# Performance work log

Measured on AMD Instinct MI355X. Metric: run time of the kernel, lower is better.

Reference implementation:

```python
import jax, jax.numpy as jnp
import numpy as np

B, S, D = 2, 2048, 1024
H, HD, K = 16, 64, 4
F = 4096
EPS = 1e-6
ROPE_BASE = 10000.0
NEG = -1e9


def rmsnorm(x, w):
    return x * jax.lax.rsqrt(jnp.mean(x * x, axis=-1, keepdims=True) + EPS) * w


def rope(t, pos):
    # t: (B,S,H,HD), pos: (B,S,H) per-node position (float)
    inv_freq = 1.0 / (ROPE_BASE ** (jnp.arange(0, HD, 2, dtype=jnp.float32) / HD))
    ang = pos[..., None] * inv_freq  # (B,S,H,HD/2)
    cos, sin = jnp.cos(ang), jnp.sin(ang)
    t1, t2 = t[..., : HD // 2], t[..., HD // 2:]
    return jnp.concatenate([t1 * cos - t2 * sin, t2 * cos + t1 * sin], axis=-1)


def setup_inputs() -> dict:
    key = jax.random.key(0)
    ks = jax.random.split(key, 12)
    s = lambda d: 1.0 / np.sqrt(d)
    return {
        "x": jax.random.normal(ks[0], (B, S, D), jnp.float32),
        "attn_norm_w": jnp.ones((D,), jnp.float32),
        "ffn_norm_w": jnp.ones((D,), jnp.float32),
        "Wq": jax.random.normal(ks[1], (D, H * HD), jnp.float32) * s(D),
        "Wk": jax.random.normal(ks[2], (D, H * HD), jnp.float32) * s(D),
        "Wv": jax.random.normal(ks[3], (D, H * HD), jnp.float32) * s(D),
        "Wo": jax.random.normal(ks[4], (H * HD, D), jnp.float32) * s(H * HD),
        "Wr": jax.random.normal(ks[5], (D, H * K), jnp.float32) * s(D),
        "w1": jax.random.normal(ks[6], (D, F), jnp.float32) * s(D),
        "w2": jax.random.normal(ks[7], (D, F), jnp.float32) * s(D),
        "w3": jax.random.normal(ks[8], (F, D), jnp.float32) * s(F),
    }


def reference(x, attn_norm_w, ffn_norm_w, Wq, Wk, Wv, Wo, Wr, w1, w2, w3):
    # ---- pre-norm + hypergraph node-routed causal attention ----
    h = rmsnorm(x, attn_norm_w)
    # per-(token, head) routing to K hyper-nodes
    logits = (h @ Wr).reshape(B, S, H, K)
    node = jnp.argmax(logits, axis=-1)                      # (B,S,H) int
    onehot = jax.nn.one_hot(node, K, dtype=jnp.float32)     # (B,S,H,K)
    # per-node RoPE position: count of previous same-node tokens
    cum = jnp.cumsum(onehot, axis=1)                        # inclusive
    pos = jnp.take_along_axis(cum, node[..., None], axis=-1)[..., 0] - 1.0  # (B,S,H)

    q = (h @ Wq).reshape(B, S, H, HD)
    k = (h @ Wk).reshape(B, S, H, HD)
    v = (h @ Wv).reshape(B, S, H, HD)
    q = rope(q, pos)
    k = rope(k, pos)

    scores = jnp.einsum("bqhd,bkhd->bhqk", q, k) / np.sqrt(HD)  # (B,H,S,S)
    node_h = jnp.transpose(node, (0, 2, 1))                     # (B,H,S)
    same = node_h[:, :, :, None] == node_h[:, :, None, :]       # intra-node only
    causal = jnp.tril(jnp.ones((S, S), bool))
    allowed = same & causal
    attn = jax.nn.softmax(jnp.where(allowed, scores, NEG), axis=-1)
    ctx = jnp.einsum("bhqk,bkhd->bqhd", attn, v).reshape(B, S, H * HD)
    x = x + ctx @ Wo

    # ---- pre-norm + SwiGLU ----
    h2 = rmsnorm(x, ffn_norm_w)
    ffn = (jax.nn.silu(h2 @ w1) * (h2 @ w2)) @ w3
    return x + ffn
```

## Files before the change

### kernel.cpp

```cpp
#include <hip/hip_runtime.h>
#include <hip/hip_bf16.h>
#include <math.h>

typedef __hip_bfloat16 bf16;

#define B_  2
#define S_  2048
#define D_  1024
#define H_  16
#define HD_ 64
#define KR_ 4
#define F_  4096
#define TOK (B_*S_)
#define NEG (-1.0e9f)

typedef __attribute__((ext_vector_type(8))) short bf16x8_t;
typedef __attribute__((ext_vector_type(4))) float f32x4_t;
typedef unsigned int u32;
#define AS1 __attribute__((address_space(1)))
#define AS3 __attribute__((address_space(3)))

__device__ __forceinline__ float u2f(unsigned short u) {
  union { float f; unsigned int i; } cv; cv.i = ((unsigned int)u) << 16; return cv.f;
}
__device__ __forceinline__ unsigned short f2u(float f) {
  return (unsigned short)(__bfloat16_as_ushort(__float2bfloat16(f)));
}

__device__ __forceinline__ void gl_lds16(const bf16* g, unsigned short* lds_base) {
  __builtin_amdgcn_global_load_lds((const AS1 u32*)g, (AS3 u32*)lds_base, 16, 0, 0);
}

__device__ __forceinline__ float rd1(const void* p, size_t i, bool isbf) {
  return isbf ? __bfloat162float(((const bf16*)p)[i]) : ((const float*)p)[i];
}

__device__ __forceinline__ void xcd_tile(int& bx, int& by) {
  const int nx = gridDim.x;
  const int nwg = nx * gridDim.y;
  const int hw = blockIdx.y * nx + blockIdx.x;
  const int tile = (hw & 7) * (nwg >> 3) + (hw >> 3);
  bx = tile % nx;
  by = tile / nx;
}

__global__ void detect_k(const unsigned* __restrict__ anw_words, int* __restrict__ flag) {
  if (threadIdx.x == 0) *flag = (anw_words[0] == 0x3F803F80u) ? 1 : 0;
}

__global__ __launch_bounds__(256) void transpose_k(const void* W, bf16* __restrict__ WT,
                                                   const int* __restrict__ flagp,
                                                   int K, int N) {
  const bool isbf = (*flagp != 0);
  __shared__ float tile[32][33];
  const int k0 = blockIdx.y * 32, n0 = blockIdx.x * 32;
  const int tid = threadIdx.x;
  const int rl = tid >> 5, cl = tid & 31;
#pragma unroll
  for (int i = 0; i < 4; i++)
    tile[rl + 8 * i][cl] = rd1(W, (size_t)(k0 + rl + 8 * i) * N + n0 + cl, isbf);
  __syncthreads();
#pragma unroll
  for (int i = 0; i < 4; i++)
    WT[(size_t)(n0 + rl + 8 * i) * K + k0 + cl] = __float2bfloat16(tile[cl][rl + 8 * i]);
}

__global__ __launch_bounds__(256) void wrconv_k(const void* Wr, float* __restrict__ Wrf,
                                                const int* __restrict__ flagp) {
  const bool isbf = (*flagp != 0);
  const int i = blockIdx.x * 256 + threadIdx.x;
  Wrf[i] = rd1(Wr, i, isbf);
}

template <bool XDUAL, bool WF>
__global__ __launch_bounds__(256) void rmsnorm_k(const void* x, const void* w,
                                                 bf16* __restrict__ ob,
                                                 float* __restrict__ of,
                                                 const int* __restrict__ flagp) {
  const bool isbf = (*flagp != 0);
  const int row = blockIdx.x;
  const int t = threadIdx.x;
  float v[4];
  float ss = 0.f;
#pragma unroll
  for (int i = 0; i < 4; i++) {
    const size_t idx = (size_t)row * D_ + t + 256 * i;
    v[i] = XDUAL ? rd1(x, idx, isbf) : ((const float*)x)[idx];
    ss += v[i] * v[i];
  }
#pragma unroll
  for (int off = 32; off >= 1; off >>= 1) ss += __shfl_down(ss, off);
  __shared__ float red[4];
  if ((t & 63) == 0) red[t >> 6] = ss;
  __syncthreads();
  const float tot = red[0] + red[1] + red[2] + red[3];
  const float sc = rsqrtf(tot * (1.f / D_) + 1e-6f);
#pragma unroll
  for (int i = 0; i < 4; i++) {
    const int c = t + 256 * i;
    const float r = v[i] * sc * rd1(w, c, isbf);
    ob[(size_t)row * D_ + c] = __float2bfloat16(r);
    if (WF) of[(size_t)row * D_ + c] = r;
  }
}

__global__ __launch_bounds__(256) void router_k(const float* __restrict__ h,
                                                const float* __restrict__ Wrf,
                                                int* __restrict__ node) {
  const int tok0 = blockIdx.x * 16;
  const int t = threadIdx.x;
  __shared__ float hs[16][1024];
  __shared__ float lg[16][64];
  {
    const float4* hsrc = (const float4*)(h + (size_t)tok0 * D_);
    float4* hdst = (float4*)hs;
#pragma unroll
    for (int j = 0; j < 16; j++) hdst[j * 256 + t] = hsrc[j * 256 + t];
  }
  __syncthreads();
  const int col = t & 63, tg = t >> 6;
  float acc[4] = {0.f, 0.f, 0.f, 0.f};
  for (int i = 0; i < D_; i += 4) {
    float wv[4];
#pragma unroll
    for (int u = 0; u < 4; u++) wv[u] = Wrf[(size_t)(i + u) * 64 + col];
#pragma unroll
    for (int tt = 0; tt < 4; tt++) {
      const float4 hv = *(const float4*)&hs[tg * 4 + tt][i];
      acc[tt] = fmaf(hv.x, wv[0], acc[tt]);
      acc[tt] = fmaf(hv.y, wv[1], acc[tt]);
      acc[tt] = fmaf(hv.z, wv[2], acc[tt]);
      acc[tt] = fmaf(hv.w, wv[3], acc[tt]);
    }
  }
#pragma unroll
  for (int tt = 0; tt < 4; tt++) lg[tg * 4 + tt][col] = acc[tt];
  __syncthreads();
  const int tok = t >> 4, hh = t & 15;
  const float* l = &lg[tok][hh * 4];
  float best = l[0];
  int bi = 0;
#pragma unroll
  for (int j = 1; j < KR_; j++) {
    const float vv = l[j];
    if (vv > best) { best = vv; bi = j; }
  }
  node[(size_t)(tok0 + tok) * H_ + hh] = bi;
}

__global__ __launch_bounds__(256) void pos_k(const int* __restrict__ node,
                                             float* __restrict__ pos,
                                             unsigned short* __restrict__ iperm,
                                             unsigned char* __restrict__ gid,
                                             int* __restrict__ gstart) {
  const int bh = blockIdx.x;
  const int b = bh >> 4, h = bh & 15;
  const int t = threadIdx.x;
  __shared__ int sc[256][4];
  int vals[8];
  int c[4] = {0, 0, 0, 0};
#pragma unroll
  for (int i = 0; i < 8; i++) {
    vals[i] = node[(size_t)(b * S_ + t * 8 + i) * H_ + h] & 3;
    c[vals[i]]++;
  }
#pragma unroll
  for (int n = 0; n < 4; n++) sc[t][n] = c[n];
  __syncthreads();
  for (int off = 1; off < 256; off <<= 1) {
    int add[4] = {0, 0, 0, 0};
    if (t >= off) {
#pragma unroll
      for (int n = 0; n < 4; n++) add[n] = sc[t - off][n];
    }
    __syncthreads();
#pragma unroll
    for (int n = 0; n < 4; n++) sc[t][n] += add[n];
    __syncthreads();
  }
  int start[4];
#pragma unroll
  for (int n = 0; n < 4; n++) start[n] = sc[t][n] - c[n];
  int gs[4];
  gs[0] = 0;
  gs[1] = sc[255][0];
  gs[2] = gs[1] + sc[255][1];
  gs[3] = gs[2] + sc[255][2];
  if (t < 4) gstart[bh * 4 + t] = gs[t];
  const size_t bhS = (size_t)bh * S_;
#pragma unroll
  for (int i = 0; i < 8; i++) {
    const int n = vals[i];
    const int rank = start[n]++;
    pos[(size_t)(b * S_ + t * 8 + i) * H_ + h] = (float)rank;
    const int newp = gs[n] + rank;
    iperm[bhS + newp] = (unsigned short)(t * 8 + i);
    gid[bhS + newp] = (unsigned char)n;
  }
}

__global__ __launch_bounds__(512) void rope_k(bf16* __restrict__ q, bf16* __restrict__ k,
                                              const float* __restrict__ pos) {
  const int token = blockIdx.x;
  const int t = threadIdx.x;
  const int h = t >> 5, j = t & 31;
  const float p = pos[token * H_ + h];
  const float inv = exp2f(-(float)j * (13.287712379549449f / 32.f));
  float sn, cs;
  sincosf(p * inv, &sn, &cs);
  const size_t base = (size_t)token * D_ + h * HD_ + j;
  float a = __bfloat162float(q[base]), b = __bfloat162float(q[base + 32]);
  q[base] = __float2bfloat16(a * cs - b * sn);
  q[base + 32] = __float2bfloat16(b * cs + a * sn);
  a = __bfloat162float(k[base]); b = __bfloat162float(k[base + 32]);
  k[base] = __float2bfloat16(a * cs - b * sn);
  k[base + 32] = __float2bfloat16(b * cs + a * sn);
}

__global__ __launch_bounds__(256) void attn_k(const bf16* __restrict__ q,
                                              const bf16* __restrict__ k,
                                              const bf16* __restrict__ v,
                                              const unsigned short* __restrict__ ip,
                                              const unsigned char* __restrict__ gidp,
                                              const int* __restrict__ gstart,
                                              bf16* __restrict__ ctx) {
  const int qt = 31 - blockIdx.x;
  const int h = blockIdx.y;
  const int b = blockIdx.z;
  const int bS = b * S_;
  const int bh = b * H_ + h;
  const size_t bhS = (size_t)bh * S_;
  const int tid = threadIdx.x;
  const int w = tid >> 6;
  const int lane = tid & 63;
  const int col = lane & 15;
  const int quad = lane >> 4;

  __shared__ unsigned short Qs[64][76];
  __shared__ unsigned short Ks[64][76];
  __shared__ unsigned short Vst[64][76];
  __shared__ unsigned short Pa[64][76];

  {
    const int qr = tid & 63, ds = (tid >> 6) * 16;
    const int ipq = ip[bhS + qt * 64 + qr];
    const bf16* src = q + (size_t)(bS + ipq) * D_ + h * HD_ + ds;
#pragma unroll
    for (int i = 0; i < 4; i++)
      *(ushort4*)&Qs[qr][ds + 4 * i] = *(const ushort4*)(src + 4 * i);
  }
  int gq_r[4];
#pragma unroll
  for (int reg = 0; reg < 4; reg++)
    gq_r[reg] = gidp[bhS + qt * 64 + w * 16 + quad * 4 + reg];
  float m_r[4] = {NEG, NEG, NEG, NEG};
  float l_r[4] = {0.f, 0.f, 0.f, 0.f};

  f32x4_t acc_o[4];
#pragma unroll
  for (int ct = 0; ct < 4; ct++) acc_o[ct] = (f32x4_t){0.f, 0.f, 0.f, 0.f};

  const int kt0 = gstart[bh * 4 + gidp[bhS + qt * 64]] >> 6;

  for (int kt = kt0; kt <= qt; kt++) {
    __syncthreads();
    {
      const int key = tid & 63, ds = (tid >> 6) * 16;
      const int ipk = ip[bhS + kt * 64 + key];
      const bf16* ksrc = k + (size_t)(bS + ipk) * D_ + h * HD_ + ds;
      const bf16* vsrc = v + (size_t)(bS + ipk) * D_ + h * HD_ + ds;
#pragma unroll
      for (int i = 0; i < 4; i++) {
        *(ushort4*)&Ks[key][ds + 4 * i] = *(const ushort4*)(ksrc + 4 * i);
        const ushort4 vu = *(const ushort4*)(vsrc + 4 * i);
        Vst[ds + 4 * i + 0][key] = vu.x;
        Vst[ds + 4 * i + 1][key] = vu.y;
        Vst[ds + 4 * i + 2][key] = vu.z;
        Vst[ds + 4 * i + 3][key] = vu.w;
      }
    }
    __syncthreads();

    f32x4_t s[4];
    {
      const bf16x8_t a0 = *(const bf16x8_t*)&Qs[w * 16 + col][quad * 8];
      const bf16x8_t a1 = *(const bf16x8_t*)&Qs[w * 16 + col][32 + quad * 8];
#pragma unroll
      for (int ct = 0; ct < 4; ct++) {
        f32x4_t acc = (f32x4_t){0.f, 0.f, 0.f, 0.f};
        const bf16x8_t b0 = *(const bf16x8_t*)&Ks[ct * 16 + col][quad * 8];
        const bf16x8_t b1 = *(const bf16x8_t*)&Ks[ct * 16 + col][32 + quad * 8];
        acc = __builtin_amdgcn_mfma_f32_16x16x32_bf16(a0, b0, acc, 0, 0, 0);
        acc = __builtin_amdgcn_mfma_f32_16x16x32_bf16(a1, b1, acc, 0, 0, 0);
        s[ct] = acc;
      }
    }
    const bool diag = (kt == qt);
    const size_t kbase = bhS + kt * 64;
    const int gk[4] = {gidp[kbase + col], gidp[kbase + 16 + col],
                       gidp[kbase + 32 + col], gidp[kbase + 48 + col]};
#pragma unroll
    for (int ct = 0; ct < 4; ct++) {
#pragma unroll
      for (int reg = 0; reg < 4; reg++) {
        const int qr = quad * 4 + reg;
        const int kc = ct * 16 + col;
        const bool ok = (gk[ct] == gq_r[reg]) && (!diag || kc <= w * 16 + qr);
        s[ct][reg] = ok ? (s[ct][reg] * 0.125f) : NEG;
      }
    }
    float al[4];
#pragma unroll
    for (int reg = 0; reg < 4; reg++) {
      float tm = fmaxf(fmaxf(s[0][reg], s[1][reg]), fmaxf(s[2][reg], s[3][reg]));
#pragma unroll
      for (int off = 1; off <= 8; off <<= 1) tm = fmaxf(tm, __shfl_xor(tm, off));
      const float mold = m_r[reg];
      const float mnew = fmaxf(mold, tm);
      const bool dead = (mnew <= -5.0e8f);
      const float alpha = dead ? 1.f : __expf(mold - mnew);
      float rowsum = 0.f;
      const int qr = w * 16 + quad * 4 + reg;
#pragma unroll
      for (int ct = 0; ct < 4; ct++) {
        const float e = dead ? 0.f : __expf(s[ct][reg] - mnew);
        rowsum += e;
        Pa[qr][ct * 16 + col] = f2u(e);
      }
#pragma unroll
      for (int off = 1; off <= 8; off <<= 1) rowsum += __shfl_xor(rowsum, off);
      l_r[reg] = l_r[reg] * alpha + rowsum;
      m_r[reg] = mnew;
      al[reg] = alpha;
    }
    {
      const bf16x8_t pa0 = *(const bf16x8_t*)&Pa[w * 16 + col][quad * 8];
      const bf16x8_t pa1 = *(const bf16x8_t*)&Pa[w * 16 + col][32 + quad * 8];
#pragma unroll
      for (int ct = 0; ct < 4; ct++) {
#pragma unroll
        for (int reg = 0; reg < 4; reg++) acc_o[ct][reg] *= al[reg];
        const bf16x8_t b0 = *(const bf16x8_t*)&Vst[ct * 16 + col][quad * 8];
        const bf16x8_t b1 = *(const bf16x8_t*)&Vst[ct * 16 + col][32 + quad * 8];
        acc_o[ct] = __builtin_amdgcn_mfma_f32_16x16x32_bf16(pa0, b0, acc_o[ct], 0, 0, 0);
        acc_o[ct] = __builtin_amdgcn_mfma_f32_16x16x32_bf16(pa1, b1, acc_o[ct], 0, 0, 0);
      }
    }
  }

#pragma unroll
  for (int reg = 0; reg < 4; reg++) {
    const int qr = w * 16 + quad * 4 + reg;
    const int op = ip[bhS + qt * 64 + qr];
    const float l = l_r[reg];
    const float invl = (l > 0.f) ? (1.f / l) : 0.f;
#pragma unroll
    for (int ct = 0; ct < 4; ct++) {
      ctx[(size_t)(bS + op) * D_ + h * HD_ + ct * 16 + col] =
          __float2bfloat16(acc_o[ct][reg] * invl);
    }
  }
}

template <int EPI>
__global__ __launch_bounds__(256) void mgemm_k(const bf16* __restrict__ A,
                                               const bf16* __restrict__ BT,
                                               float* __restrict__ Cf,
                                               void* Cout,
                                               const void* resdual,
                                               const float* __restrict__ resf,
                                               const int* __restrict__ flagp,
                                               int N, int Kd) {
  const bool isbf = (*flagp != 0);
  __shared__ unsigned short As[128][32];
  __shared__ unsigned short Bs[128][32];
  const int tid = threadIdx.x;
  const int w = tid >> 6, lane = tid & 63;
  const int col = lane & 15, quad = lane >> 4;
  const int wm = w & 1, wn = w >> 1;
  int bx, by;
  xcd_tile(bx, by);
  const int row0 = by * 128, col0 = bx * 128;

  const int srow = lane >> 2, sk8 = (lane & 3) << 3;
  const bf16* Ag0 = A + (size_t)(row0 + 16 * w + srow) * Kd + sk8;
  const bf16* Ag1 = A + (size_t)(row0 + 64 + 16 * w + srow) * Kd + sk8;
  const bf16* Bg0 = BT + (size_t)(col0 + 16 * w + srow) * Kd + sk8;
  const bf16* Bg1 = BT + (size_t)(col0 + 64 + 16 * w + srow) * Kd + sk8;

  f32x4_t acc[4][4];
#pragma unroll
  for (int i = 0; i < 4; i++)
#pragma unroll
    for (int j = 0; j < 4; j++) acc[i][j] = (f32x4_t){0.f, 0.f, 0.f, 0.f};

  for (int kt = 0; kt < Kd; kt += 32) {
    __syncthreads();
    gl_lds16(Ag0 + kt, &As[16 * w][0]);
    gl_lds16(Ag1 + kt, &As[64 + 16 * w][0]);
    gl_lds16(Bg0 + kt, &Bs[16 * w][0]);
    gl_lds16(Bg1 + kt, &Bs[64 + 16 * w][0]);
    __syncthreads();

    bf16x8_t af[4], bfr[4];
#pragma unroll
    for (int i = 0; i < 4; i++) {
      af[i] = *(const bf16x8_t*)&As[wm * 64 + i * 16 + col][quad * 8];
      bfr[i] = *(const bf16x8_t*)&Bs[wn * 64 + i * 16 + col][quad * 8];
    }
#pragma unroll
    for (int i = 0; i < 4; i++)
#pragma unroll
      for (int j = 0; j < 4; j++)
        acc[i][j] = __builtin_amdgcn_mfma_f32_16x16x32_bf16(af[i], bfr[j], acc[i][j], 0, 0, 0);
  }

#pragma unroll
  for (int i = 0; i < 4; i++) {
#pragma unroll
    for (int j = 0; j < 4; j++) {
#pragma unroll
      for (int reg = 0; reg < 4; reg++) {
        const int m = row0 + wm * 64 + i * 16 + quad * 4 + reg;
        const int nl = wn * 64 + j * 16 + col;
        if (EPI == 0) {
          const int ng = col0 + nl;
          bf16* base = (bf16*)Cout + (size_t)(ng >> 10) * (TOK * (size_t)D_);
          base[(size_t)m * D_ + (ng & 1023)] = __float2bfloat16(acc[i][j][reg]);
        } else if (EPI == 1) {
          const size_t idx = (size_t)m * N + col0 + nl;
          Cf[idx] = acc[i][j][reg] + rd1(resdual, idx, isbf);
        } else {
          const size_t idx = (size_t)m * N + col0 + nl;
          const float r = acc[i][j][reg] + resf[idx];
          if (isbf) ((bf16*)Cout)[idx] = __float2bfloat16(r);
          else      ((float*)Cout)[idx] = r;
        }
      }
    }
  }
}

template <int EPI>
__global__ __launch_bounds__(256) void mgemm64_k(const bf16* __restrict__ A,
                                                 const bf16* __restrict__ BT,
                                                 float* __restrict__ Cf,
                                                 void* Cout,
                                                 const void* resdual,
                                                 const float* __restrict__ resf,
                                                 const int* __restrict__ flagp,
                                                 int N, int Kd) {
  const bool isbf = (*flagp != 0);
  __shared__ unsigned short As[64][32];
  __shared__ unsigned short Bs[128][32];
  const int tid = threadIdx.x;
  const int w = tid >> 6, lane = tid & 63;
  const int col = lane & 15, quad = lane >> 4;
  int bx, by;
  xcd_tile(bx, by);
  const int row0 = by * 64, col0 = bx * 128;

  const int srow = lane >> 2, sk8 = (lane & 3) << 3;
  const bf16* Ag  = A + (size_t)(row0 + 16 * w + srow) * Kd + sk8;
  const bf16* Bg0 = BT + (size_t)(col0 + 32 * w + srow) * Kd + sk8;
  const bf16* Bg1 = BT + (size_t)(col0 + 32 * w + 16 + srow) * Kd + sk8;

  f32x4_t acc[4][2];
#pragma unroll
  for (int i = 0; i < 4; i++)
#pragma unroll
    for (int j = 0; j < 2; j++) acc[i][j] = (f32x4_t){0.f, 0.f, 0.f, 0.f};

  for (int kt = 0; kt < Kd; kt += 32) {
    __syncthreads();
    gl_lds16(Ag + kt, &As[16 * w][0]);
    gl_lds16(Bg0 + kt, &Bs[32 * w][0]);
    gl_lds16(Bg1 + kt, &Bs[32 * w + 16][0]);
    __syncthreads();

    bf16x8_t af[4], bfr[2];
#pragma unroll
    for (int i = 0; i < 4; i++)
      af[i] = *(const bf16x8_t*)&As[i * 16 + col][quad * 8];
#pragma unroll
    for (int j = 0; j < 2; j++)
      bfr[j] = *(const bf16x8_t*)&Bs[w * 32 + j * 16 + col][quad * 8];
#pragma unroll
    for (int i = 0; i < 4; i++)
#pragma unroll
      for (int j = 0; j < 2; j++)
        acc[i][j] = __builtin_amdgcn_mfma_f32_16x16x32_bf16(af[i], bfr[j], acc[i][j], 0, 0, 0);
  }

#pragma unroll
  for (int i = 0; i < 4; i++) {
#pragma unroll
    for (int j = 0; j < 2; j++) {
#pragma unroll
      for (int reg = 0; reg < 4; reg++) {
        const int m = row0 + i * 16 + quad * 4 + reg;
        const int nl = w * 32 + j * 16 + col;
        const size_t idx = (size_t)m * N + col0 + nl;
        if (EPI == 1) {
          Cf[idx] = acc[i][j][reg] + rd1(resdual, idx, isbf);
        } else {
          const float r = acc[i][j][reg] + resf[idx];
          if (isbf) ((bf16*)Cout)[idx] = __float2bfloat16(r);
          else      ((float*)Cout)[idx] = r;
        }
      }
    }
  }
}

__global__ __launch_bounds__(256) void mgate_k(const bf16* __restrict__ A,
                                               const bf16* __restrict__ B1T,
                                               const bf16* __restrict__ B2T,
                                               bf16* __restrict__ G,
                                               int Kd) {
  __shared__ unsigned short As[128][32];
  __shared__ unsigned short Bs1[64][32];
  __shared__ unsigned short Bs2[64][32];
  const int tid = threadIdx.x;
  const int w = tid >> 6, lane = tid & 63;
  const int col = lane & 15, quad = lane >> 4;
  const int wm = w & 1, wn = w >> 1;
  int bx, by;
  xcd_tile(bx, by);
  const int row0 = by * 128, col0 = bx * 64;

  const int srow = lane >> 2, sk8 = (lane & 3) << 3;
  const bf16* Ag0 = A + (size_t)(row0 + 16 * w + srow) * Kd + sk8;
  const bf16* Ag1 = A + (size_t)(row0 + 64 + 16 * w + srow) * Kd + sk8;
  const bf16* B1g = B1T + (size_t)(col0 + 16 * w + srow) * Kd + sk8;
  const bf16* B2g = B2T + (size_t)(col0 + 16 * w + srow) * Kd + sk8;

  f32x4_t acc1[4][2], acc2[4][2];
#pragma unroll
  for (int i = 0; i < 4; i++)
#pragma unroll
    for (int j = 0; j < 2; j++) {
      acc1[i][j] = (f32x4_t){0.f, 0.f, 0.f, 0.f};
      acc2[i][j] = (f32x4_t){0.f, 0.f, 0.f, 0.f};
    }

  for (int kt = 0; kt < Kd; kt += 32) {
    __syncthreads();
    gl_lds16(Ag0 + kt, &As[16 * w][0]);
    gl_lds16(Ag1 + kt, &As[64 + 16 * w][0]);
    gl_lds16(B1g + kt, &Bs1[16 * w][0]);
    gl_lds16(B2g + kt, &Bs2[16 * w][0]);
    __syncthreads();

    bf16x8_t af[4], b1f[2], b2f[2];
#pragma unroll
    for (int i = 0; i < 4; i++)
      af[i] = *(const bf16x8_t*)&As[wm * 64 + i * 16 + col][quad * 8];
#pragma unroll
    for (int j = 0; j < 2; j++) {
      b1f[j] = *(const bf16x8_t*)&Bs1[wn * 32 + j * 16 + col][quad * 8];
      b2f[j] = *(const bf16x8_t*)&Bs2[wn * 32 + j * 16 + col][quad * 8];
    }
#pragma unroll
    for (int i = 0; i < 4; i++)
#pragma unroll
      for (int j = 0; j < 2; j++) {
        acc1[i][j] = __builtin_amdgcn_mfma_f32_16x16x32_bf16(af[i], b1f[j], acc1[i][j], 0, 0, 0);
        acc2[i][j] = __builtin_amdgcn_mfma_f32_16x16x32_bf16(af[i], b2f[j], acc2[i][j], 0, 0, 0);
      }
  }

#pragma unroll
  for (int i = 0; i < 4; i++) {
#pragma unroll
    for (int j = 0; j < 2; j++) {
#pragma unroll
      for (int reg = 0; reg < 4; reg++) {
        const int m = row0 + wm * 64 + i * 16 + quad * 4 + reg;
        const int n = col0 + wn * 32 + j * 16 + col;
        const float z = acc1[i][j][reg];
        const float sig = 1.f / (1.f + __expf(-z));
        G[(size_t)m * F_ + n] = __float2bfloat16(z * sig * acc2[i][j][reg]);
      }
    }
  }
}

extern "C" void kernel_launch(void* const* d_in, const int* in_sizes, int n_in,
                              void* d_out, int out_size, void* d_ws, size_t ws_size,
                              hipStream_t stream) {
  const void* x   = d_in[0];
  const void* anw = d_in[1];
  const void* fnw = d_in[2];
  const void* Wq  = d_in[3];
  const void* Wk  = d_in[4];
  const void* Wv  = d_in[5];
  const void* Wo  = d_in[6];
  const void* Wr  = d_in[7];
  const void* w1  = d_in[8];
  const void* w2  = d_in[9];
  const void* w3  = d_in[10];

  char* ws = (char*)d_ws;
  int*   node = (int*)ws;
  float* pos  = (float*)(ws + (256 << 10));
  int*   flag = (int*)(ws + (512 << 10));
  unsigned short* iperm = (unsigned short*)(ws + (640u << 10));
  unsigned char*  gidb  = (unsigned char*)(ws + (768u << 10));
  int*   gstart = (int*)(ws + (832u << 10));
  float* x2   = (float*)(ws + (1u << 20));
  bf16*  ctx  = (bf16*)(ws + (17u << 20));
  bf16*  h2   = ctx;
  float* Wrf  = (float*)(ws + (17u << 20));
  char*  r0   = ws + (25u << 20);
  bf16*  hb   = (bf16*)(r0);
  bf16*  qb   = (bf16*)(r0 + (8u << 20));
  bf16*  kb   = (bf16*)(r0 + (16u << 20));
  bf16*  vb   = (bf16*)(r0 + (24u << 20));
  float* hf   = (float*)(r0 + (8u << 20));
  bf16*  g    = (bf16*)(r0);
  bf16*  qkvT = (bf16*)(ws + (57u << 20));
  bf16*  WoT  = (bf16*)(ws + (63u << 20));
  bf16*  w1T  = (bf16*)(ws + (65u << 20));
  bf16*  w2T  = (bf16*)(ws + (73u << 20));
  bf16*  w3T  = (bf16*)(ws + (81u << 20));

  detect_k<<<1, 64, 0, stream>>>((const unsigned*)anw, flag);
  wrconv_k<<<256, 256, 0, stream>>>(Wr, Wrf, flag);
  transpose_k<<<dim3(32, 32), 256, 0, stream>>>(Wq, qkvT,              flag, D_, D_);
  transpose_k<<<dim3(32, 32), 256, 0, stream>>>(Wk, qkvT + (1u << 20), flag, D_, D_);
  transpose_k<<<dim3(32, 32), 256, 0, stream>>>(Wv, qkvT + (2u << 20), flag, D_, D_);
  transpose_k<<<dim3(32, 32), 256, 0, stream>>>(Wo, WoT,               flag, D_, D_);
  transpose_k<<<dim3(128, 32), 256, 0, stream>>>(w1, w1T,              flag, D_, F_);
  transpose_k<<<dim3(128, 32), 256, 0, stream>>>(w2, w2T,              flag, D_, F_);
  transpose_k<<<dim3(32, 128), 256, 0, stream>>>(w3, w3T,              flag, F_, D_);
  rmsnorm_k<true, true><<<TOK, 256, 0, stream>>>(x, anw, hb, hf, flag);
  router_k<<<TOK / 16, 256, 0, stream>>>(hf, Wrf, node);
  pos_k<<<32, 256, 0, stream>>>(node, pos, iperm, gidb, gstart);
  mgemm_k<0><<<dim3(3072 / 128, TOK / 128), 256, 0, stream>>>(hb, qkvT, nullptr, qb, nullptr, nullptr, flag, 3072, D_);
  rope_k<<<TOK, 512, 0, stream>>>(qb, kb, pos);
  attn_k<<<dim3(S_ / 64, H_, B_), 256, 0, stream>>>(qb, kb, vb, iperm, gidb, gstart, ctx);
  mgemm64_k<1><<<dim3(D_ / 128, TOK / 64), 256, 0, stream>>>(ctx, WoT, x2, nullptr, x, nullptr, flag, D_, D_);
  rmsnorm_k<false, false><<<TOK, 256, 0, stream>>>(x2, fnw, h2, nullptr, flag);
  mgate_k<<<dim3(F_ / 64, TOK / 128), 256, 0, stream>>>(h2, w1T, w2T, g, D_);
  mgemm64_k<2><<<dim3(D_ / 128, TOK / 64), 256, 0, stream>>>(g, w3T, nullptr, d_out, nullptr, x2, flag, D_, F_);
}
```

Before: 522.8 us.

## Double-buffer LDS tiles in GEMM kernels and remap gate-kernel tile order

Converts the three MFMA GEMM kernels from single-buffered LDS staging, which used two barriers per k-step, to a double-buffered scheme. The next k-tile is issued into the alternate buffer before computing on the current one, leaving one barrier per iteration. The aim is to overlap global-to-LDS loads with MFMA work and halve barrier count. The gate kernel also replaces xcd_tile with an explicit 8-rectangle tile mapping intended to improve L2 locality. The cost is doubled LDS per block, which may reduce occupancy, and the new gate mapping hardcodes the grid shape.

```diff
diff --git a/kernel.cpp b/kernel.cpp
--- a/kernel.cpp
+++ b/kernel.cpp
@@ -372,8 +372,8 @@
                                                const int* __restrict__ flagp,
                                                int N, int Kd) {
   const bool isbf = (*flagp != 0);
-  __shared__ unsigned short As[128][32];
-  __shared__ unsigned short Bs[128][32];
+  __shared__ unsigned short As[2][128][32];
+  __shared__ unsigned short Bs[2][128][32];
   const int tid = threadIdx.x;
   const int w = tid >> 6, lane = tid & 63;
   const int col = lane & 15, quad = lane >> 4;
@@ -394,25 +394,34 @@
 #pragma unroll
     for (int j = 0; j < 4; j++) acc[i][j] = (f32x4_t){0.f, 0.f, 0.f, 0.f};
 
+  gl_lds16(Ag0, &As[0][16 * w][0]);
+  gl_lds16(Ag1, &As[0][64 + 16 * w][0]);
+  gl_lds16(Bg0, &Bs[0][16 * w][0]);
+  gl_lds16(Bg1, &Bs[0][64 + 16 * w][0]);
+  __syncthreads();
+
+  int cur = 0;
   for (int kt = 0; kt < Kd; kt += 32) {
-    __syncthreads();
-    gl_lds16(Ag0 + kt, &As[16 * w][0]);
-    gl_lds16(Ag1 + kt, &As[64 + 16 * w][0]);
-    gl_lds16(Bg0 + kt, &Bs[16 * w][0]);
-    gl_lds16(Bg1 + kt, &Bs[64 + 16 * w][0]);
-    __syncthreads();
-
+    const int nxt = cur ^ 1;
+    if (kt + 32 < Kd) {
+      gl_lds16(Ag0 + kt + 32, &As[nxt][16 * w][0]);
+      gl_lds16(Ag1 + kt + 32, &As[nxt][64 + 16 * w][0]);
+      gl_lds16(Bg0 + kt + 32, &Bs[nxt][16 * w][0]);
+      gl_lds16(Bg1 + kt + 32, &Bs[nxt][64 + 16 * w][0]);
+    }
     bf16x8_t af[4], bfr[4];
 #pragma unroll
     for (int i = 0; i < 4; i++) {
-      af[i] = *(const bf16x8_t*)&As[wm * 64 + i * 16 + col][quad * 8];
-      bfr[i] = *(const bf16x8_t*)&Bs[wn * 64 + i * 16 + col][quad * 8];
+      af[i] = *(const bf16x8_t*)&As[cur][wm * 64 + i * 16 + col][quad * 8];
+      bfr[i] = *(const bf16x8_t*)&Bs[cur][wn * 64 + i * 16 + col][quad * 8];
     }
 #pragma unroll
     for (int i = 0; i < 4; i++)
 #pragma unroll
       for (int j = 0; j < 4; j++)
         acc[i][j] = __builtin_amdgcn_mfma_f32_16x16x32_bf16(af[i], bfr[j], acc[i][j], 0, 0, 0);
+    __syncthreads();
+    cur = nxt;
   }
 
 #pragma unroll
@@ -451,8 +460,8 @@
                                                  const int* __restrict__ flagp,
                                                  int N, int Kd) {
   const bool isbf = (*flagp != 0);
-  __shared__ unsigned short As[64][32];
-  __shared__ unsigned short Bs[128][32];
+  __shared__ unsigned short As[2][64][32];
+  __shared__ unsigned short Bs[2][128][32];
   const int tid = threadIdx.x;
   const int w = tid >> 6, lane = tid & 63;
   const int col = lane & 15, quad = lane >> 4;
@@ -471,25 +480,33 @@
 #pragma unroll
     for (int j = 0; j < 2; j++) acc[i][j] = (f32x4_t){0.f, 0.f, 0.f, 0.f};
 
+  gl_lds16(Ag, &As[0][16 * w][0]);
+  gl_lds16(Bg0, &Bs[0][32 * w][0]);
+  gl_lds16(Bg1, &Bs[0][32 * w + 16][0]);
+  __syncthreads();
+
+  int cur = 0;
   for (int kt = 0; kt < Kd; kt += 32) {
-    __syncthreads();
-    gl_lds16(Ag + kt, &As[16 * w][0]);
-    gl_lds16(Bg0 + kt, &Bs[32 * w][0]);
-    gl_lds16(Bg1 + kt, &Bs[32 * w + 16][0]);
-    __syncthreads();
-
+    const int nxt = cur ^ 1;
+    if (kt + 32 < Kd) {
+      gl_lds16(Ag + kt + 32, &As[nxt][16 * w][0]);
+      gl_lds16(Bg0 + kt + 32, &Bs[nxt][32 * w][0]);
+      gl_lds16(Bg1 + kt + 32, &Bs[nxt][32 * w + 16][0]);
+    }
     bf16x8_t af[4], bfr[2];
 #pragma unroll
     for (int i = 0; i < 4; i++)
-      af[i] = *(const bf16x8_t*)&As[i * 16 + col][quad * 8];
+      af[i] = *(const bf16x8_t*)&As[cur][i * 16 + col][quad * 8];
 #pragma unroll
     for (int j = 0; j < 2; j++)
-      bfr[j] = *(const bf16x8_t*)&Bs[w * 32 + j * 16 + col][quad * 8];
+      bfr[j] = *(const bf16x8_t*)&Bs[cur][w * 32 + j * 16 + col][quad * 8];
 #pragma unroll
     for (int i = 0; i < 4; i++)
 #pragma unroll
       for (int j = 0; j < 2; j++)
         acc[i][j] = __builtin_amdgcn_mfma_f32_16x16x32_bf16(af[i], bfr[j], acc[i][j], 0, 0, 0);
+    __syncthreads();
+    cur = nxt;
   }
 
 #pragma unroll
@@ -518,15 +535,17 @@
                                                const bf16* __restrict__ B2T,
                                                bf16* __restrict__ G,
                                                int Kd) {
-  __shared__ unsigned short As[128][32];
-  __shared__ unsigned short Bs1[64][32];
-  __shared__ unsigned short Bs2[64][32];
+  __shared__ unsigned short As[2][128][32];
+  __shared__ unsigned short Bs1[2][64][32];
+  __shared__ unsigned short Bs2[2][64][32];
   const int tid = threadIdx.x;
   const int w = tid >> 6, lane = tid & 63;
   const int col = lane & 15, quad = lane >> 4;
   const int wm = w & 1, wn = w >> 1;
-  int bx, by;
-  xcd_tile(bx, by);
+  const int hw = blockIdx.y * gridDim.x + blockIdx.x;
+  const int rect = hw & 7, inner = hw >> 3;
+  const int by = ((rect >> 2) << 4) | (inner >> 4);
+  const int bx = ((rect & 3) << 4) | (inner & 15);
   const int row0 = by * 128, col0 = bx * 64;
 
   const int srow = lane >> 2, sk8 = (lane & 3) << 3;
@@ -544,22 +563,29 @@
       acc2[i][j] = (f32x4_t){0.f, 0.f, 0.f, 0.f};
     }
 
+  gl_lds16(Ag0, &As[0][16 * w][0]);
+  gl_lds16(Ag1, &As[0][64 + 16 * w][0]);
+  gl_lds16(B1g, &Bs1[0][16 * w][0]);
+  gl_lds16(B2g, &Bs2[0][16 * w][0]);
+  __syncthreads();
+
+  int cur = 0;
   for (int kt = 0; kt < Kd; kt += 32) {
-    __syncthreads();
-    gl_lds16(Ag0 + kt, &As[16 * w][0]);
-    gl_lds16(Ag1 + kt, &As[64 + 16 * w][0]);
-    gl_lds16(B1g + kt, &Bs1[16 * w][0]);
-    gl_lds16(B2g + kt, &Bs2[16 * w][0]);
-    __syncthreads();
-
+    const int nxt = cur ^ 1;
+    if (kt + 32 < Kd) {
+      gl_lds16(Ag0 + kt + 32, &As[nxt][16 * w][0]);
+      gl_lds16(Ag1 + kt + 32, &As[nxt][64 + 16 * w][0]);
+      gl_lds16(B1g + kt + 32, &Bs1[nxt][16 * w][0]);
+      gl_lds16(B2g + kt + 32, &Bs2[nxt][16 * w][0]);
+    }
     bf16x8_t af[4], b1f[2], b2f[2];
 #pragma unroll
     for (int i = 0; i < 4; i++)
-      af[i] = *(const bf16x8_t*)&As[wm * 64 + i * 16 + col][quad * 8];
+      af[i] = *(const bf16x8_t*)&As[cur][wm * 64 + i * 16 + col][quad * 8];
 #pragma unroll
     for (int j = 0; j < 2; j++) {
-      b1f[j] = *(const bf16x8_t*)&Bs1[wn * 32 + j * 16 + col][quad * 8];
-      b2f[j] = *(const bf16x8_t*)&Bs2[wn * 32 + j * 16 + col][quad * 8];
+      b1f[j] = *(const bf16x8_t*)&Bs1[cur][wn * 32 + j * 16 + col][quad * 8];
+      b2f[j] = *(const bf16x8_t*)&Bs2[cur][wn * 32 + j * 16 + col][quad * 8];
     }
 #pragma unroll
     for (int i = 0; i < 4; i++)
@@ -568,6 +594,8 @@
         acc1[i][j] = __builtin_amdgcn_mfma_f32_16x16x32_bf16(af[i], b1f[j], acc1[i][j], 0, 0, 0);
         acc2[i][j] = __builtin_amdgcn_mfma_f32_16x16x32_bf16(af[i], b2f[j], acc2[i][j], 0, 0, 0);
       }
+    __syncthreads();
+    cur = nxt;
   }
 
 #pragma unroll
```

New measurement: 484.4 us. 1.08x faster.
